# Performance work log

Hardware: AMD Instinct MI355X
Metric: run time of the kernel (lower is better)

Reference implementation:

```python
import jax, jax.numpy as jnp
import numpy as np

B, S, H, NH = 2, 2048, 1024, 16
HD = H // NH  # head_dim = 64


def setup_inputs() -> dict:
    key = jax.random.key(0)
    kx, kl, kq, kk, kv, ko = jax.random.split(key, 6)
    scale = 1.0 / np.sqrt(H)
    return {
        "x": jax.random.normal(kx, (B, S, H), dtype=jnp.float32),
        "seq_lengths": jax.random.randint(kl, (B,), 1, S + 1, dtype=jnp.int32),
        "Wq": jax.random.normal(kq, (H, H), dtype=jnp.float32) * scale,
        "Wk": jax.random.normal(kk, (H, H), dtype=jnp.float32) * scale,
        "Wv": jax.random.normal(kv, (H, H), dtype=jnp.float32) * scale,
        "Wo": jax.random.normal(ko, (H, H), dtype=jnp.float32) * scale,
    }


def reference(x, seq_lengths, Wq, Wk, Wv, Wo):
    b, s, _ = x.shape
    # projections (nn.Linear with no bias: x @ W.T)
    q = (x @ Wq.T).reshape(b, s, NH, HD).transpose(0, 2, 1, 3)  # [b,h,s,d]
    k = (x @ Wk.T).reshape(b, s, NH, HD).transpose(0, 2, 1, 3)
    v = (x @ Wv.T).reshape(b, s, NH, HD).transpose(0, 2, 1, 3)

    scores = jnp.einsum("bhqd,bhkd->bhqk", q, k) / jnp.sqrt(jnp.float32(HD))

    causal = jnp.triu(jnp.ones((s, s), dtype=bool), k=1)[None, None]  # [1,1,s,s]
    padding = (jnp.arange(s)[None, :] >= seq_lengths[:, None])[:, None, None, :]
    mask = causal | padding
    scores = jnp.where(mask, -jnp.inf, scores)

    att = jax.nn.softmax(scores, axis=-1)  # stable: subtract row max once
    out = jnp.einsum("bhqk,bhkd->bhqd", att, v)
    out = out.transpose(0, 2, 1, 3).reshape(b, s, H)
    return out @ Wo.T
```

## Files before the change

### kernel.cpp

```cpp
#include <hip/hip_runtime.h>

typedef unsigned short u16;
typedef short bf16x8 __attribute__((ext_vector_type(8)));
typedef float f32x4 __attribute__((ext_vector_type(4)));

#define DEVINL __device__ __forceinline__

DEVINL u16 f2bf(float f) {
    union { float f; unsigned int u; } x;
    x.f = f;
    unsigned int u = x.u;
    unsigned int r = (u + 0x7fffu + ((u >> 16) & 1u)) >> 16;
    return (u16)r;
}

DEVINL u16 f2bf_fast(float f) {
    union { float f; unsigned int u; } x;
    x.f = f;
    return (u16)((x.u + 0x8000u) >> 16);
}

DEVINL void async16(const u16* g, u16* l) {
    __builtin_amdgcn_global_load_lds(
        (const __attribute__((address_space(1))) void*)g,
        (__attribute__((address_space(3))) void*)l, 16, 0, 0);
}

DEVINL void store_out(u16* p, float v)   { *p = f2bf(v); }
DEVINL void store_out(float* p, float v) { *p = v; }

__global__ void pma_cvt_kernel(const float* __restrict__ in, u16* __restrict__ out, int n4) {
    int i = blockIdx.x * blockDim.x + threadIdx.x;
    if (i < n4) {
        float4 v = reinterpret_cast<const float4*>(in)[i];
        ushort4 o;
        o.x = f2bf(v.x); o.y = f2bf(v.y); o.z = f2bf(v.z); o.w = f2bf(v.w);
        reinterpret_cast<ushort4*>(out)[i] = o;
    }
}

__global__ void pma_cvt4_kernel(const float* __restrict__ w0, const float* __restrict__ w1,
                                const float* __restrict__ w2, const float* __restrict__ w3,
                                u16* __restrict__ dst) {
    const int wsel = blockIdx.y;
    const float* in = (wsel == 0) ? w0 : (wsel == 1) ? w1 : (wsel == 2) ? w2 : w3;
    u16* out = dst + (size_t)wsel * 1024 * 1024;
    const float s = (wsel == 0) ? 0.125f : 1.0f;
    int i = blockIdx.x * blockDim.x + threadIdx.x;
    float4 v = reinterpret_cast<const float4*>(in)[i];
    ushort4 o;
    o.x = f2bf(v.x * s); o.y = f2bf(v.y * s); o.z = f2bf(v.z * s); o.w = f2bf(v.w * s);
    reinterpret_cast<ushort4*>(out)[i] = o;
}

template <typename OutT>
__global__ __launch_bounds__(256) void pma_gemm_bt(
    const u16* __restrict__ A,
    const u16* __restrict__ W0, const u16* __restrict__ W1, const u16* __restrict__ W2,
    OutT* __restrict__ O0, OutT* __restrict__ O1, OutT* __restrict__ O2,
    int K, int nbn_per, int vtr_which,
    const int* __restrict__ seq_lengths, int skip_kv)
{
    const int t = threadIdx.x;
    const int lane = t & 63, wave = t >> 6;
    const int m0 = blockIdx.x * 128;
    const int bn = blockIdx.y;
    const int which = bn / nbn_per;
    const int n0 = (bn % nbn_per) * 128;

    if (skip_kv && which != 0) {
        if ((m0 & 2047) >= seq_lengths[m0 >> 11]) return;
    }

    const u16* W = (which == 0) ? W0 : (which == 1) ? W1 : W2;
    OutT* O = (which == 0) ? O0 : (which == 1) ? O1 : O2;

    __shared__ u16 Alds[128 * 32];
    __shared__ u16 Blds[128 * 32];

    const int wm = wave >> 1, wn = wave & 1;
    const int r16 = lane & 15, g4 = lane >> 4;

    f32x4 acc[4][4];
    const f32x4 z = {0.f, 0.f, 0.f, 0.f};
#pragma unroll
    for (int m = 0; m < 4; ++m)
#pragma unroll
        for (int n = 0; n < 4; ++n) acc[m][n] = z;

    for (int k0 = 0; k0 < K; k0 += 32) {
        __syncthreads();
#pragma unroll
        for (int j = 0; j < 2; ++j) {
            int i = j * 256 + t;
            int row = i >> 2, seg = i & 3;
            async16(A + (size_t)(m0 + row) * K + k0 + seg * 8,
                    Alds + (size_t)(j * 256 + wave * 64) * 8);
            async16(W + (size_t)(n0 + row) * K + k0 + seg * 8,
                    Blds + (size_t)(j * 256 + wave * 64) * 8);
        }
        __syncthreads();

        bf16x8 af[4], bfr[4];
#pragma unroll
        for (int m = 0; m < 4; ++m)
            af[m] = *reinterpret_cast<const bf16x8*>(Alds + (wm * 64 + m * 16 + r16) * 32 + g4 * 8);
#pragma unroll
        for (int n = 0; n < 4; ++n)
            bfr[n] = *reinterpret_cast<const bf16x8*>(Blds + (wn * 64 + n * 16 + r16) * 32 + g4 * 8);
#pragma unroll
        for (int m = 0; m < 4; ++m)
#pragma unroll
            for (int n = 0; n < 4; ++n)
                acc[m][n] = __builtin_amdgcn_mfma_f32_16x16x32_bf16(af[m], bfr[n], acc[m][n], 0, 0, 0);
    }

    bool vtr = false;
    if constexpr (sizeof(OutT) == 2) vtr = (which == vtr_which);
    if (vtr) {
        if constexpr (sizeof(OutT) == 2) {
#pragma unroll
            for (int m = 0; m < 4; ++m)
#pragma unroll
                for (int n = 0; n < 4; ++n) {
                    int row = m0 + wm * 64 + m * 16 + g4 * 4;
                    int col = n0 + wn * 64 + n * 16 + r16;
                    ushort4 pk;
                    pk.x = f2bf(acc[m][n][0]); pk.y = f2bf(acc[m][n][1]);
                    pk.z = f2bf(acc[m][n][2]); pk.w = f2bf(acc[m][n][3]);
                    size_t addr = ((size_t)((row >> 11) * 16 + (col >> 6)) * 64 + (col & 63)) * 2048
                                  + (row & 2047);
                    *reinterpret_cast<ushort4*>((u16*)O + addr) = pk;
                }
        }
    } else {
#pragma unroll
        for (int m = 0; m < 4; ++m)
#pragma unroll
            for (int n = 0; n < 4; ++n) {
                int row = m0 + wm * 64 + m * 16 + g4 * 4;
                int col = n0 + wn * 64 + n * 16 + r16;
#pragma unroll
                for (int r = 0; r < 4; ++r)
                    store_out(&O[(size_t)(row + r) * 1024 + col], acc[m][n][r]);
            }
    }
}

__global__ __launch_bounds__(256, 4) void pma_attn_kernel(
    const u16* __restrict__ Q, const u16* __restrict__ Kp, const u16* __restrict__ Vt,
    const int* __restrict__ seq_lengths, u16* __restrict__ O)
{
    const int bx = blockIdx.x;
    const int qt = 31 - (bx >> 5);
    const int bh = bx & 31;
    const int h  = bh & 15;
    const int b  = bh >> 4;
    const int q0 = qt * 64;
    const int t = threadIdx.x, lane = t & 63, w = t >> 6;
    const int r16 = lane & 15, g4 = lane >> 4;
    const int seqlen = seq_lengths[b];
    const float L2E = 1.4426950408889634f;

    __shared__ u16 Klds[64 * 72];
    __shared__ u16 Vtlds[64 * 72];
    __shared__ u16 Plds[64 * 72];

    const size_t bbase = (size_t)b * 2048 * 1024;
    const size_t hoff = (size_t)h * 64;
    const size_t vrow0 = (size_t)((b * 16 + h) * 64);

    const f32x4 z = {0.f, 0.f, 0.f, 0.f};
    const int krel = t >> 3;
    const int seg  = t & 7;

    const size_t qrowbase = bbase + (size_t)(q0 + w * 16 + r16) * 1024 + hoff;
    const bf16x8 qf0 = *reinterpret_cast<const bf16x8*>(Q + qrowbase + g4 * 8);
    const bf16x8 qf1 = *reinterpret_cast<const bf16x8*>(Q + qrowbase + 32 + g4 * 8);

    f32x4 acc[4];
#pragma unroll
    for (int f = 0; f < 4; ++f) acc[f] = z;
    float mrow = -1e30f, lrow = 0.f;

    int kmax = q0 + 63;
    if (seqlen - 1 < kmax) kmax = seqlen - 1;
    const int nt = (kmax >> 6) + 1;

    const u16* kbase = Kp + bbase + hoff + (size_t)krel * 1024 + seg * 8;
    const u16* vbase = Vt + (vrow0 + krel) * 2048 + seg * 8;

    bf16x8 kreg[2], vreg[2];

#pragma unroll
    for (int j = 0; j < 2; ++j) {
        kreg[j] = *reinterpret_cast<const bf16x8*>(kbase + j * 32 * 1024);
        vreg[j] = *reinterpret_cast<const bf16x8*>(vbase + j * 32 * 2048);
    }
#pragma unroll
    for (int j = 0; j < 2; ++j) {
        const int rr = j * 32 + krel;
        *reinterpret_cast<bf16x8*>(Klds + rr * 72 + seg * 8) = kreg[j];
        *reinterpret_cast<bf16x8*>(Vtlds + rr * 72 + seg * 8) = vreg[j];
    }
    __syncthreads();

    const int qhat = q0 + w * 16 + r16;

    for (int tt = 0; tt < nt; ++tt) {
        const int t0 = tt << 6;

        if (tt + 1 < nt) {
            const int t0n = (tt + 1) << 6;
#pragma unroll
            for (int j = 0; j < 2; ++j) {
                kreg[j] = *reinterpret_cast<const bf16x8*>(kbase + (size_t)t0n * 1024 + j * 32 * 1024);
                vreg[j] = *reinterpret_cast<const bf16x8*>(vbase + t0n + j * 32 * 2048);
            }
        }

        f32x4 sraw[4];
        __builtin_amdgcn_s_setprio(1);
#pragma unroll
        for (int kc = 0; kc < 4; ++kc) {
            bf16x8 kf0 = *reinterpret_cast<const bf16x8*>(Klds + (kc * 16 + r16) * 72 + g4 * 8);
            bf16x8 kf1 = *reinterpret_cast<const bf16x8*>(Klds + (kc * 16 + r16) * 72 + 32 + g4 * 8);
            f32x4 s = z;
            s = __builtin_amdgcn_mfma_f32_16x16x32_bf16(kf0, qf0, s, 0, 0, 0);
            s = __builtin_amdgcn_mfma_f32_16x16x32_bf16(kf1, qf1, s, 0, 0, 0);
            sraw[kc] = s;
        }
        __builtin_amdgcn_s_setprio(0);

        float sc[4][4];
        const bool needmask = (t0 == q0) || (t0 + 64 > seqlen);
        if (needmask) {
#pragma unroll
            for (int kc = 0; kc < 4; ++kc) {
                const int keyb = t0 + kc * 16 + g4 * 4;
#pragma unroll
                for (int r = 0; r < 4; ++r)
                    sc[kc][r] = ((keyb + r > qhat) || (keyb + r >= seqlen)) ? -1e30f : sraw[kc][r];
            }
        } else {
#pragma unroll
            for (int kc = 0; kc < 4; ++kc)
#pragma unroll
                for (int r = 0; r < 4; ++r) sc[kc][r] = sraw[kc][r];
        }

        float mx;
        {
            float m0 = fmaxf(fmaxf(sc[0][0], sc[0][1]), fmaxf(sc[0][2], sc[0][3]));
            float m1 = fmaxf(fmaxf(sc[1][0], sc[1][1]), fmaxf(sc[1][2], sc[1][3]));
            float m2 = fmaxf(fmaxf(sc[2][0], sc[2][1]), fmaxf(sc[2][2], sc[2][3]));
            float m3 = fmaxf(fmaxf(sc[3][0], sc[3][1]), fmaxf(sc[3][2], sc[3][3]));
            mx = fmaxf(fmaxf(m0, m1), fmaxf(m2, m3));
        }
        mx = fmaxf(mx, __shfl_xor(mx, 16, 64));
        mx = fmaxf(mx, __shfl_xor(mx, 32, 64));

        const bool norescale = __all(mx <= mrow + 8.0f);
        float mnew, corr;
        if (norescale) { mnew = mrow; corr = 1.0f; }
        else           { mnew = fmaxf(mrow, mx); corr = exp2f((mrow - mnew) * L2E); }

        const float nb = mnew * L2E;
#pragma unroll
        for (int kc = 0; kc < 4; ++kc)
#pragma unroll
            for (int r = 0; r < 4; ++r)
                sc[kc][r] = exp2f(__builtin_fmaf(sc[kc][r], L2E, -nb));
        float rs;
        {
            float s0 = (sc[0][0] + sc[0][1]) + (sc[0][2] + sc[0][3]);
            float s1 = (sc[1][0] + sc[1][1]) + (sc[1][2] + sc[1][3]);
            float s2 = (sc[2][0] + sc[2][1]) + (sc[2][2] + sc[2][3]);
            float s3 = (sc[3][0] + sc[3][1]) + (sc[3][2] + sc[3][3]);
            rs = (s0 + s1) + (s2 + s3);
        }
        rs += __shfl_xor(rs, 16, 64);
        rs += __shfl_xor(rs, 32, 64);
        lrow = lrow * corr + rs;
        mrow = mnew;

#pragma unroll
        for (int kc = 0; kc < 4; ++kc) {
            ushort4 pk;
            pk.x = f2bf_fast(sc[kc][0]); pk.y = f2bf_fast(sc[kc][1]);
            pk.z = f2bf_fast(sc[kc][2]); pk.w = f2bf_fast(sc[kc][3]);
            *reinterpret_cast<ushort4*>(Plds + (w * 16 + r16) * 72 + kc * 16 + g4 * 4) = pk;
        }

        if (!norescale) {
            float cr0 = __shfl(corr, g4 * 4 + 0, 64);
            float cr1 = __shfl(corr, g4 * 4 + 1, 64);
            float cr2 = __shfl(corr, g4 * 4 + 2, 64);
            float cr3 = __shfl(corr, g4 * 4 + 3, 64);
#pragma unroll
            for (int f = 0; f < 4; ++f) {
                f32x4 a = acc[f];
                a[0] *= cr0; a[1] *= cr1; a[2] *= cr2; a[3] *= cr3;
                acc[f] = a;
            }
        }

        __builtin_amdgcn_s_setprio(1);
#pragma unroll
        for (int kc2 = 0; kc2 < 2; ++kc2) {
            bf16x8 pa = *reinterpret_cast<const bf16x8*>(Plds + (w * 16 + r16) * 72 + kc2 * 32 + g4 * 8);
#pragma unroll
            for (int f = 0; f < 4; ++f) {
                bf16x8 vb = *reinterpret_cast<const bf16x8*>(Vtlds + (f * 16 + r16) * 72 + kc2 * 32 + g4 * 8);
                acc[f] = __builtin_amdgcn_mfma_f32_16x16x32_bf16(pa, vb, acc[f], 0, 0, 0);
            }
        }
        __builtin_amdgcn_s_setprio(0);
        __syncthreads();

        if (tt + 1 < nt) {
#pragma unroll
            for (int j = 0; j < 2; ++j) {
                const int rr = j * 32 + krel;
                *reinterpret_cast<bf16x8*>(Klds + rr * 72 + seg * 8) = kreg[j];
                *reinterpret_cast<bf16x8*>(Vtlds + rr * 72 + seg * 8) = vreg[j];
            }
            __syncthreads();
        }
    }

    {
        float lr0 = __shfl(lrow, g4 * 4 + 0, 64);
        float lr1 = __shfl(lrow, g4 * 4 + 1, 64);
        float lr2 = __shfl(lrow, g4 * 4 + 2, 64);
        float lr3 = __shfl(lrow, g4 * 4 + 3, 64);
        float lr[4] = {lr0, lr1, lr2, lr3};
#pragma unroll
        for (int f = 0; f < 4; ++f)
#pragma unroll
            for (int r = 0; r < 4; ++r) {
                int sr = q0 + w * 16 + g4 * 4 + r;
                float o = acc[f][r] / lr[r];
                O[bbase + (size_t)sr * 1024 + hoff + f * 16 + r16] = f2bf(o);
            }
    }
}

extern "C" void kernel_launch(void* const* d_in, const int* in_sizes, int n_in,
                              void* d_out, int out_size, void* d_ws, size_t ws_size,
                              hipStream_t stream) {
    const float* x   = (const float*)d_in[0];
    const int*   sql = (const int*)d_in[1];
    const float* Wq  = (const float*)d_in[2];
    const float* Wk  = (const float*)d_in[3];
    const float* Wv  = (const float*)d_in[4];
    const float* Wo  = (const float*)d_in[5];
    float* out = (float*)d_out;

    const size_t MB = 1024 * 1024;
    char* ws = (char*)d_ws;
    u16* xb   = (u16*)(ws + 0 * MB);
    u16* wqb  = (u16*)(ws + 8 * MB);
    u16* wkb  = (u16*)(ws + 10 * MB);
    u16* wvb  = (u16*)(ws + 12 * MB);
    u16* wob  = (u16*)(ws + 14 * MB);
    u16* Qb   = (u16*)(ws + 16 * MB);
    u16* Kb   = (u16*)(ws + 24 * MB);
    u16* Vtb  = (u16*)(ws + 32 * MB);
    u16* attb = (u16*)(ws + 40 * MB);

    pma_cvt_kernel<<<4096, 256, 0, stream>>>(x, xb, 1048576);
    pma_cvt4_kernel<<<dim3(1024, 4), 256, 0, stream>>>(Wq, Wk, Wv, Wo, wqb);

    pma_gemm_bt<u16><<<dim3(32, 24), 256, 0, stream>>>(xb, wqb, wkb, wvb, Qb, Kb, Vtb,
                                                       1024, 8, 2, sql, 1);

    pma_attn_kernel<<<1024, 256, 0, stream>>>(Qb, Kb, Vtb, sql, attb);

    pma_gemm_bt<float><<<dim3(32, 8), 256, 0, stream>>>(attb, wob, wob, wob, out, out, out,
                                                        1024, 8, -1, sql, 0);
}
```

Measured before the change: 125.3 us.

## Double-buffer K/V tiles in LDS with XOR swizzle, drop per-tile barrier

K and V tiles are now held in two LDS buffers that alternate by tile parity. The next tile is written into the idle buffer, which removes the __syncthreads that followed the P·V MFMAs, leaving one barrier per iteration. Row padding (stride 72) is replaced by an XOR swizzle of 16-byte chunks at stride 64 for K, V and P, meant to avoid bank conflicts without the padding waste. The cost is more LDS per block (about 40KB versus about 27KB), which may press on occupancy at four blocks per CU, plus some extra index arithmetic.

Result: faster. 120.8 us (-3.6%).

```diff
diff --git a/kernel.cpp b/kernel.cpp
--- a/kernel.cpp
+++ b/kernel.cpp
@@ -162,9 +162,9 @@
     const int seqlen = seq_lengths[b];
     const float L2E = 1.4426950408889634f;
 
-    __shared__ u16 Klds[64 * 72];
-    __shared__ u16 Vtlds[64 * 72];
-    __shared__ u16 Plds[64 * 72];
+    __shared__ u16 Klds[2 * 64 * 64];
+    __shared__ u16 Vlds[2 * 64 * 64];
+    __shared__ u16 Plds[64 * 64];
 
     const size_t bbase = (size_t)b * 2048 * 1024;
     const size_t hoff = (size_t)h * 64;
@@ -189,6 +189,12 @@
 
     const u16* kbase = Kp + bbase + hoff + (size_t)krel * 1024 + seg * 8;
     const u16* vbase = Vt + (vrow0 + krel) * 2048 + seg * 8;
+    const int stw = krel * 64 + ((seg ^ (krel & 7)) * 8);
+
+    const int r7 = r16 & 7;
+    const int kread_lo = r16 * 64 + ((g4 ^ r7) * 8);
+    const int kread_hi = r16 * 64 + (((g4 + 4) ^ r7) * 8);
+    const int prow = (w * 16 + r16) * 64;
 
     bf16x8 kreg[2], vreg[2];
 
@@ -199,9 +205,8 @@
     }
 #pragma unroll
     for (int j = 0; j < 2; ++j) {
-        const int rr = j * 32 + krel;
-        *reinterpret_cast<bf16x8*>(Klds + rr * 72 + seg * 8) = kreg[j];
-        *reinterpret_cast<bf16x8*>(Vtlds + rr * 72 + seg * 8) = vreg[j];
+        *reinterpret_cast<bf16x8*>(Klds + stw + j * 2048) = kreg[j];
+        *reinterpret_cast<bf16x8*>(Vlds + stw + j * 2048) = vreg[j];
     }
     __syncthreads();
 
@@ -209,6 +214,8 @@
 
     for (int tt = 0; tt < nt; ++tt) {
         const int t0 = tt << 6;
+        const int dbo = (tt & 1) << 12;
+        const int dbn = 4096 - dbo;
 
         if (tt + 1 < nt) {
             const int t0n = (tt + 1) << 6;
@@ -223,8 +230,8 @@
         __builtin_amdgcn_s_setprio(1);
 #pragma unroll
         for (int kc = 0; kc < 4; ++kc) {
-            bf16x8 kf0 = *reinterpret_cast<const bf16x8*>(Klds + (kc * 16 + r16) * 72 + g4 * 8);
-            bf16x8 kf1 = *reinterpret_cast<const bf16x8*>(Klds + (kc * 16 + r16) * 72 + 32 + g4 * 8);
+            bf16x8 kf0 = *reinterpret_cast<const bf16x8*>(Klds + dbo + kc * 1024 + kread_lo);
+            bf16x8 kf1 = *reinterpret_cast<const bf16x8*>(Klds + dbo + kc * 1024 + kread_hi);
             f32x4 s = z;
             s = __builtin_amdgcn_mfma_f32_16x16x32_bf16(kf0, qf0, s, 0, 0, 0);
             s = __builtin_amdgcn_mfma_f32_16x16x32_bf16(kf1, qf1, s, 0, 0, 0);
@@ -289,7 +296,8 @@
             ushort4 pk;
             pk.x = f2bf_fast(sc[kc][0]); pk.y = f2bf_fast(sc[kc][1]);
             pk.z = f2bf_fast(sc[kc][2]); pk.w = f2bf_fast(sc[kc][3]);
-            *reinterpret_cast<ushort4*>(Plds + (w * 16 + r16) * 72 + kc * 16 + g4 * 4) = pk;
+            const int phys16 = (kc * 2 + (g4 >> 1)) ^ r7;
+            *reinterpret_cast<ushort4*>(Plds + prow + phys16 * 8 + (g4 & 1) * 4) = pk;
         }
 
         if (!norescale) {
@@ -308,22 +316,21 @@
         __builtin_amdgcn_s_setprio(1);
 #pragma unroll
         for (int kc2 = 0; kc2 < 2; ++kc2) {
-            bf16x8 pa = *reinterpret_cast<const bf16x8*>(Plds + (w * 16 + r16) * 72 + kc2 * 32 + g4 * 8);
+            bf16x8 pa = *reinterpret_cast<const bf16x8*>(Plds + prow + (((kc2 * 4 + g4) ^ r7) * 8));
 #pragma unroll
             for (int f = 0; f < 4; ++f) {
-                bf16x8 vb = *reinterpret_cast<const bf16x8*>(Vtlds + (f * 16 + r16) * 72 + kc2 * 32 + g4 * 8);
+                bf16x8 vb = *reinterpret_cast<const bf16x8*>(
+                    Vlds + dbo + (f * 16 + r16) * 64 + (((kc2 * 4 + g4) ^ r7) * 8));
                 acc[f] = __builtin_amdgcn_mfma_f32_16x16x32_bf16(pa, vb, acc[f], 0, 0, 0);
             }
         }
         __builtin_amdgcn_s_setprio(0);
-        __syncthreads();
 
         if (tt + 1 < nt) {
 #pragma unroll
             for (int j = 0; j < 2; ++j) {
-                const int rr = j * 32 + krel;
-                *reinterpret_cast<bf16x8*>(Klds + rr * 72 + seg * 8) = kreg[j];
-                *reinterpret_cast<bf16x8*>(Vtlds + rr * 72 + seg * 8) = vreg[j];
+                *reinterpret_cast<bf16x8*>(Klds + dbn + stw + j * 2048) = kreg[j];
+                *reinterpret_cast<bf16x8*>(Vlds + dbn + stw + j * 2048) = vreg[j];
             }
             __syncthreads();
         }
```
